# Performance work log

Measured on AMD Instinct MI355X. Metric: run time of the kernel, lower is better.

Reference implementation:

```python
import jax, jax.numpy as jnp
import numpy as np

FS = 44100
N_SINES = 1000
RESAMPLE = 32
TWO_PI = 2.0 * np.pi


def _linear_upsample(x, scale):
    """Match torch F.interpolate(mode='linear', align_corners=False).
    x: [B, C, N] -> [B, C, N*scale]"""
    n = x.shape[-1]
    out_n = n * scale
    # source coordinate for each output sample
    coords = (jnp.arange(out_n, dtype=jnp.float32) + 0.5) / scale - 0.5
    coords = jnp.clip(coords, 0.0, n - 1)
    lo = jnp.floor(coords).astype(jnp.int32)
    hi = jnp.minimum(lo + 1, n - 1)
    w = (coords - lo.astype(jnp.float32)).astype(x.dtype)
    return x[..., lo] * (1.0 - w) + x[..., hi] * w


def setup_inputs() -> dict:
    key = jax.random.key(0)
    k1, k2 = jax.random.split(key)
    B, S, F = 4, N_SINES, 256
    frequencies = jax.random.uniform(k1, (B, S, F), dtype=jnp.float32) * 5000.0 + 40.0
    amplitudes = jax.random.uniform(k2, (B, S, F), dtype=jnp.float32) / N_SINES
    init_phases = jnp.zeros((B, S), dtype=jnp.float32)
    return {"frequencies": frequencies, "amplitudes": amplitudes, "init_phases": init_phases}


def reference(frequencies, amplitudes, init_phases):
    freqs = _linear_upsample(frequencies, RESAMPLE)
    amps = _linear_upsample(amplitudes, RESAMPLE)
    # angular increment per sample
    omegas = freqs * (TWO_PI / FS)
    # phase accumulation (inclusive cumsum) plus carried-in phase state
    phases = jnp.cumsum(omegas, axis=-1) + init_phases[:, :, None]
    # additive synthesis: sum over sines -> [B, 1, T]
    signal = jnp.sum(amps * jnp.sin(phases), axis=1, keepdims=True)
    return signal
```

## Files before the change

kernel.cpp:

```cpp
#include <hip/hip_runtime.h>
#include <hip/hip_fp16.h>


#define FS_D 44100.0
#define S_TOTAL 1000
#define FRAMES 256
#define T_OUT 8192
#define BATCH 4
#define CH 8
#define NC 125
#define KQ 4

template <bool ATOMIC>
__global__ __launch_bounds__(256, 8) void synth(
    const float* __restrict__ freq, const float* __restrict__ amp,
    const float* __restrict__ initp, __half* __restrict__ pdst,
    float* __restrict__ odst)
{
  __shared__ float base_lds[CH][FRAMES];
  __shared__ float head_lds[CH];
  __shared__ float4 coef_lds[CH][64];

  const int bx    = blockIdx.x;
  const int b     = bx / (NC * KQ);
  const int rem   = bx % (NC * KQ);
  const int chunk = rem >> 2;
  const int kq    = rem & 3;
  const int s0    = chunk * CH;
  const int tid   = threadIdx.x;
  const int lane  = tid & 63;
  const int wave  = tid >> 6;

  const float invfs = (float)(1.0 / FS_D);

  {
    const int kA  = kq * 64 + lane;
    const int kA1 = (kA < FRAMES - 1) ? kA + 1 : kA;
    #pragma unroll
    for (int i = 0; i < 2; ++i) {
      const int r = 2 * wave + i;
      const long long roff = (long long)(b * S_TOTAL + s0 + r) * FRAMES;
      const float fA  = freq[roff + kA];
      const float fA1 = freq[roff + kA1];
      const float aA  = amp[roff + kA];
      const float aA1 = amp[roff + kA1];
      const float c1  = fA * invfs;
      const float c2  = (fA1 - fA) * (invfs * (1.0f / 64.0f));
      const float d1  = (aA1 - aA) * (1.0f / 32.0f);
      const float a0p = fmaf(-0.5f, d1, aA);
      coef_lds[r][lane] = make_float4(c1, c2, d1, a0p);
    }
  }

  {
    const double inv2pi = 0.15915494309189535;
    const double k16    = 16.0 / FS_D;
    #pragma unroll
    for (int r = wave; r < CH; r += 4) {
      const int s = s0 + r;
      const long long roff = (long long)(b * S_TOTAL + s) * FRAMES;
      const float4 fv = reinterpret_cast<const float4*>(freq + roff)[lane];
      const double f0 = fv.x, f1 = fv.y, f2 = fv.z, f3 = fv.w;
      const double tot = f0 + f1 + f2 + f3;
      double incl = tot;
      #pragma unroll
      for (int off = 1; off < 64; off <<= 1) {
        double v = __shfl_up(incl, (unsigned)off, 64);
        if (lane >= off) incl += v;
      }
      double C = incl - tot;
      const double initrev = (double)initp[b * S_TOTAL + s] * inv2pi;
      if (lane == 0) head_lds[r] = (float)(initrev - floor(initrev));
      const double fk[4] = {f0, f1, f2, f3};
      #pragma unroll
      for (int i = 0; i < 4; ++i) {
        const double basev = k16 * (2.0 * C + fk[i]) + initrev;
        base_lds[r][4 * lane + i] = (float)(basev - floor(basev));
        C += fk[i];
      }
    }
  }
  __syncthreads();

  const int q = wave;
  const int k = kq * 64 + lane;
  const bool special = (k == FRAMES - 1);
  const bool hd      = special && (q >= 2);
  const int qq  = hd ? (q - 2) : q;
  const int j0  = qq * 8;
  const int t0  = hd ? j0 : (k * 32 + 16 + j0);

  float uu[8];
  const float u0f = (float)(j0 + 1);
  #pragma unroll
  for (int jj = 0; jj < 8; ++jj) uu[jj] = u0f + (float)jj;

  float acc[8];
  #pragma unroll
  for (int jj = 0; jj < 8; ++jj) acc[jj] = 0.f;

  #pragma unroll
  for (int r = 0; r < CH; ++r) {
    float4 cf = coef_lds[r][lane];
    float bs  = base_lds[r][k];
    if (hd) {
      const long long roff0 = (long long)(b * S_TOTAL + s0 + r) * FRAMES;
      cf.x = freq[roff0] * invfs;
      cf.y = 0.f; cf.z = 0.f;
      cf.w = amp[roff0];
      bs   = head_lds[r];
    }
    #pragma unroll
    for (int jj = 0; jj < 8; ++jj) {
      const float p  = fmaf(fmaf(cf.y, uu[jj], cf.x), uu[jj], bs);
      const float am = fmaf(cf.z, uu[jj], cf.w);
      acc[jj] = fmaf(am, __builtin_amdgcn_sinf(__builtin_amdgcn_fractf(p)), acc[jj]);
    }
  }

  if (ATOMIC) {
    float* outb = odst + (long long)b * T_OUT + t0;
    #pragma unroll
    for (int jj = 0; jj < 8; ++jj) atomicAdd(outb + jj, acc[jj]);
  } else {
    __half* pout = pdst + (size_t)(b * NC + chunk) * T_OUT + t0;
    union { float4 f; __half2 h[4]; } u;
    u.h[0] = __floats2half2_rn(acc[0], acc[1]);
    u.h[1] = __floats2half2_rn(acc[2], acc[3]);
    u.h[2] = __floats2half2_rn(acc[4], acc[5]);
    u.h[3] = __floats2half2_rn(acc[6], acc[7]);
    *reinterpret_cast<float4*>(pout) = u.f;
  }
}

__global__ __launch_bounds__(256) void reduce_out(
    const __half* __restrict__ partial, float* __restrict__ out)
{
  __shared__ float red_x[4][64];
  __shared__ float red_y[4][64];
  const int tid  = threadIdx.x;
  const int lane = tid & 63;
  const int w    = tid >> 6;
  const int i    = blockIdx.x * 64 + lane;
  const int b    = i >> 12;
  const int t2   = i & 4095;
  const __half2* p =
      reinterpret_cast<const __half2*>(partial + (size_t)b * NC * T_OUT) + t2;
  float sx = 0.f, sy = 0.f;
  #pragma unroll 8
  for (int c = w; c < NC; c += 4) {
    const float2 v = __half22float2(p[c * (T_OUT / 2)]);
    sx += v.x; sy += v.y;
  }
  red_x[w][lane] = sx;
  red_y[w][lane] = sy;
  __syncthreads();
  if (tid < 64) {
    const float ox = (red_x[0][lane] + red_x[1][lane]) +
                     (red_x[2][lane] + red_x[3][lane]);
    const float oy = (red_y[0][lane] + red_y[1][lane]) +
                     (red_y[2][lane] + red_y[3][lane]);
    reinterpret_cast<float2*>(out)[i] = make_float2(ox, oy);
  }
}

extern "C" void kernel_launch(void* const* d_in, const int* in_sizes, int n_in,
                              void* d_out, int out_size, void* d_ws, size_t ws_size,
                              hipStream_t stream) {
  const float* freq  = (const float*)d_in[0];
  const float* amp   = (const float*)d_in[1];
  const float* initp = (const float*)d_in[2];
  float* out = (float*)d_out;

  const size_t need = (size_t)BATCH * NC * T_OUT * sizeof(__half);

  if (ws_size >= need) {
    __half* partial = (__half*)d_ws;
    synth<false><<<dim3(BATCH * NC * KQ), dim3(256), 0, stream>>>(
        freq, amp, initp, partial, nullptr);
    reduce_out<<<dim3((BATCH * T_OUT / 2) / 64), dim3(256), 0, stream>>>(
        partial, out);
  } else {
    hipMemsetAsync(d_out, 0, (size_t)out_size * sizeof(float), stream);
    synth<true><<<dim3(BATCH * NC * KQ), dim3(256), 0, stream>>>(
        freq, amp, initp, nullptr, out);
  }
}
```

Baseline: 22.32 us.

## Merge frame-quarter blocks into one 1024-thread block sharing prefix scan

Each block now covers all 256 frames of a sine chunk with 16 waves, instead of four 256-thread blocks per chunk. The double-precision phase prefix scan and the coefficient setup run once per chunk rather than four times. The last-frame head case now reads an extra LDS slot instead of global memory. The cost is fewer, larger blocks and a block-wide barrier across 16 waves, which may reduce occupancy flexibility.

New measurement: 21.63 us. 1.03x faster.

```diff
diff --git a/kernel.cpp b/kernel.cpp
--- a/kernel.cpp
+++ b/kernel.cpp
@@ -9,86 +9,80 @@
 #define BATCH 4
 #define CH 8
 #define NC 125
-#define KQ 4
 
 template <bool ATOMIC>
-__global__ __launch_bounds__(256, 8) void synth(
+__global__ __launch_bounds__(1024, 8) void synth(
     const float* __restrict__ freq, const float* __restrict__ amp,
     const float* __restrict__ initp, __half* __restrict__ pdst,
     float* __restrict__ odst)
 {
-  __shared__ float base_lds[CH][FRAMES];
-  __shared__ float head_lds[CH];
-  __shared__ float4 coef_lds[CH][64];
+  __shared__ float4 coef_lds[CH][FRAMES + 1];
+  __shared__ float  base_lds[CH][FRAMES + 4];
 
   const int bx    = blockIdx.x;
-  const int b     = bx / (NC * KQ);
-  const int rem   = bx % (NC * KQ);
-  const int chunk = rem >> 2;
-  const int kq    = rem & 3;
+  const int b     = bx / NC;
+  const int chunk = bx % NC;
   const int s0    = chunk * CH;
   const int tid   = threadIdx.x;
   const int lane  = tid & 63;
-  const int wave  = tid >> 6;
+  const int w     = tid >> 6;
 
   const float invfs = (float)(1.0 / FS_D);
 
-  {
-    const int kA  = kq * 64 + lane;
+  #pragma unroll
+  for (int rr = 0; rr < 2; ++rr) {
+    const int r  = rr * 4 + (w >> 2);
+    const int kA = (w & 3) * 64 + lane;
     const int kA1 = (kA < FRAMES - 1) ? kA + 1 : kA;
-    #pragma unroll
-    for (int i = 0; i < 2; ++i) {
-      const int r = 2 * wave + i;
-      const long long roff = (long long)(b * S_TOTAL + s0 + r) * FRAMES;
-      const float fA  = freq[roff + kA];
-      const float fA1 = freq[roff + kA1];
-      const float aA  = amp[roff + kA];
-      const float aA1 = amp[roff + kA1];
-      const float c1  = fA * invfs;
-      const float c2  = (fA1 - fA) * (invfs * (1.0f / 64.0f));
-      const float d1  = (aA1 - aA) * (1.0f / 32.0f);
-      const float a0p = fmaf(-0.5f, d1, aA);
-      coef_lds[r][lane] = make_float4(c1, c2, d1, a0p);
-    }
+    const long long roff = (long long)(b * S_TOTAL + s0 + r) * FRAMES;
+    const float fA  = freq[roff + kA];
+    const float fA1 = freq[roff + kA1];
+    const float aA  = amp[roff + kA];
+    const float aA1 = amp[roff + kA1];
+    const float c1  = fA * invfs;
+    const float c2  = (fA1 - fA) * (invfs * (1.0f / 64.0f));
+    const float d1  = (aA1 - aA) * (1.0f / 32.0f);
+    const float a0p = fmaf(-0.5f, d1, aA);
+    coef_lds[r][kA] = make_float4(c1, c2, d1, a0p);
+    if (kA == 0) coef_lds[r][FRAMES] = make_float4(c1, 0.f, 0.f, aA);
   }
 
-  {
+  if (w < 8) {
+    const int r = w;
     const double inv2pi = 0.15915494309189535;
     const double k16    = 16.0 / FS_D;
+    const long long roff = (long long)(b * S_TOTAL + s0 + r) * FRAMES;
+    const float4 fv = reinterpret_cast<const float4*>(freq + roff)[lane];
+    const double f0 = fv.x, f1 = fv.y, f2 = fv.z, f3 = fv.w;
+    const double tot = f0 + f1 + f2 + f3;
+    double incl = tot;
     #pragma unroll
-    for (int r = wave; r < CH; r += 4) {
-      const int s = s0 + r;
-      const long long roff = (long long)(b * S_TOTAL + s) * FRAMES;
-      const float4 fv = reinterpret_cast<const float4*>(freq + roff)[lane];
-      const double f0 = fv.x, f1 = fv.y, f2 = fv.z, f3 = fv.w;
-      const double tot = f0 + f1 + f2 + f3;
-      double incl = tot;
-      #pragma unroll
-      for (int off = 1; off < 64; off <<= 1) {
-        double v = __shfl_up(incl, (unsigned)off, 64);
-        if (lane >= off) incl += v;
-      }
-      double C = incl - tot;
-      const double initrev = (double)initp[b * S_TOTAL + s] * inv2pi;
-      if (lane == 0) head_lds[r] = (float)(initrev - floor(initrev));
-      const double fk[4] = {f0, f1, f2, f3};
-      #pragma unroll
-      for (int i = 0; i < 4; ++i) {
-        const double basev = k16 * (2.0 * C + fk[i]) + initrev;
-        base_lds[r][4 * lane + i] = (float)(basev - floor(basev));
-        C += fk[i];
-      }
+    for (int off = 1; off < 64; off <<= 1) {
+      double v = __shfl_up(incl, (unsigned)off, 64);
+      if (lane >= off) incl += v;
     }
+    double C = incl - tot;
+    const double initrev = (double)initp[b * S_TOTAL + s0 + r] * inv2pi;
+    if (lane == 0) base_lds[r][FRAMES] = (float)(initrev - floor(initrev));
+    const double fk[4] = {f0, f1, f2, f3};
+    float4 bw;
+    #pragma unroll
+    for (int i = 0; i < 4; ++i) {
+      const double basev = k16 * (2.0 * C + fk[i]) + initrev;
+      (&bw.x)[i] = (float)(basev - floor(basev));
+      C += fk[i];
+    }
+    *reinterpret_cast<float4*>(&base_lds[r][4 * lane]) = bw;
   }
   __syncthreads();
 
-  const int q = wave;
-  const int k = kq * 64 + lane;
-  const bool special = (k == FRAMES - 1);
-  const bool hd      = special && (q >= 2);
-  const int qq  = hd ? (q - 2) : q;
-  const int j0  = qq * 8;
-  const int t0  = hd ? j0 : (k * 32 + 16 + j0);
+  const int q = w & 3;
+  const int k = (w >> 2) * 64 + lane;
+  const bool hd = (k == FRAMES - 1) && (q >= 2);
+  const int kidx = hd ? FRAMES : k;
+  const int qq = hd ? (q - 2) : q;
+  const int j0 = qq * 8;
+  const int t0 = hd ? j0 : (k * 32 + 16 + j0);
 
   float uu[8];
   const float u0f = (float)(j0 + 1);
@@ -101,15 +95,8 @@
 
   #pragma unroll
   for (int r = 0; r < CH; ++r) {
-    float4 cf = coef_lds[r][lane];
-    float bs  = base_lds[r][k];
-    if (hd) {
-      const long long roff0 = (long long)(b * S_TOTAL + s0 + r) * FRAMES;
-      cf.x = freq[roff0] * invfs;
-      cf.y = 0.f; cf.z = 0.f;
-      cf.w = amp[roff0];
-      bs   = head_lds[r];
-    }
+    const float4 cf = coef_lds[r][kidx];
+    const float  bs = base_lds[r][kidx];
     #pragma unroll
     for (int jj = 0; jj < 8; ++jj) {
       const float p  = fmaf(fmaf(cf.y, uu[jj], cf.x), uu[jj], bs);
@@ -176,13 +163,13 @@
 
   if (ws_size >= need) {
     __half* partial = (__half*)d_ws;
-    synth<false><<<dim3(BATCH * NC * KQ), dim3(256), 0, stream>>>(
+    synth<false><<<dim3(BATCH * NC), dim3(1024), 0, stream>>>(
         freq, amp, initp, partial, nullptr);
     reduce_out<<<dim3((BATCH * T_OUT / 2) / 64), dim3(256), 0, stream>>>(
         partial, out);
   } else {
     hipMemsetAsync(d_out, 0, (size_t)out_size * sizeof(float), stream);
-    synth<true><<<dim3(BATCH * NC * KQ), dim3(256), 0, stream>>>(
+    synth<true><<<dim3(BATCH * NC), dim3(1024), 0, stream>>>(
         freq, amp, initp, nullptr, out);
   }
 }
```
